# Performance work log

Hardware: AMD Instinct MI355X
Metric: run time of the kernel (lower is better)

Reference implementation:

```python
import jax, jax.numpy as jnp
import numpy as np


def setup_inputs() -> dict:
    key = jax.random.key(0)
    k1, k2, k3, k4, k5 = jax.random.split(key, 5)
    B, T, N, F, H = 32, 12, 512, 64, 64
    cat_x = jax.random.normal(k1, (B, T, N, F), dtype=jnp.float32)
    # Linear params (stored as [in, out]; torch stores [out, in] and does x @ W.T)
    lim = 1.0 / np.sqrt(F)
    Wq = jax.random.uniform(k2, (F, H), jnp.float32, -lim, lim)
    bq = jax.random.uniform(k3, (H,), jnp.float32, -lim, lim)
    Wk = jax.random.uniform(k4, (F, H), jnp.float32, -lim, lim)
    bk = jax.random.uniform(k5, (H,), jnp.float32, -lim, lim)
    return {"cat_x": cat_x, "Wq": Wq, "bq": bq, "Wk": Wk, "bk": bk, "tau": 4}


def reference(cat_x, Wq, bq, Wk, bk, tau):
    # cat_x: [B, T, N, F]
    q = cat_x @ Wq + bq  # [B, T, N, H]
    k = cat_x @ Wk + bk  # [B, T, N, H]
    qf = jnp.fft.rfft(q, axis=-1)  # [B, T, N, Fr]
    kf = jnp.fft.rfft(k, axis=-1)  # [B, T, N, Fr]
    # Vectorized over the original Python loop over i (query time step):
    # res[b, i, j, n, :] = qf[b, i, n, :] * conj(kf[b, j, n, :])
    res = qf[:, :, None, :, :] * jnp.conj(kf)[:, None, :, :, :]  # [B, Ti, Tj, N, Fr]
    corr = jnp.fft.irfft(res, axis=-1)  # [B, Ti, Tj, N, H] (H even -> exact round trip)
    # mean over batch, then hidden (last), then nodes == mean over (B, N, H)
    score_set = jnp.mean(corr, axis=(0, 3, 4))  # [Ti, Tj]
    scores, indices = jax.lax.top_k(score_set, tau)
    return scores, indices
```

## Files before the change

### kernel.cpp

```cpp
#include <hip/hip_runtime.h>

#define BB 32
#define TT 12
#define NN 512
#define FF 64
#define HH 64
#define NBLK 32
#define NCHUNK (NN / NBLK)
#define GRID (BB * NCHUNK)

#define WS_S  0
#define WS_WQ 144
#define WS_WK 208
#define WS_BQ 272
#define WS_BK 273

__global__ __launch_bounds__(384) void fft_sel_init(
    const float* __restrict__ Wq, const float* __restrict__ bq,
    const float* __restrict__ Wk, const float* __restrict__ bk,
    float* __restrict__ ws)
{
    const int tid = threadIdx.x;
    if (tid < TT * TT) {
        ws[WS_S + tid] = 0.f;
    } else if (tid >= 144 && tid < 144 + FF) {
        const int f = tid - 144;
        float a = 0.f;
        #pragma unroll
        for (int h = 0; h < HH; ++h) a += Wq[f * HH + h];
        ws[WS_WQ + f] = a;
    } else if (tid >= 208 && tid < 208 + FF) {
        const int f = tid - 208;
        float a = 0.f;
        #pragma unroll
        for (int h = 0; h < HH; ++h) a += Wk[f * HH + h];
        ws[WS_WK + f] = a;
    } else if (tid == 272) {
        float a = 0.f;
        #pragma unroll
        for (int h = 0; h < HH; ++h) a += bq[h];
        ws[WS_BQ] = a;
    } else if (tid == 273) {
        float a = 0.f;
        #pragma unroll
        for (int h = 0; h < HH; ++h) a += bk[h];
        ws[WS_BK] = a;
    }
}

__global__ __launch_bounds__(256) void fft_sel_main(
    const float* __restrict__ x,
    const float* __restrict__ ws,
    float* __restrict__ S)
{
    __shared__ float sq[TT][NBLK + 1];
    __shared__ float sk[TT][NBLK + 1];

    const int tid  = threadIdx.x;
    const int wave = tid >> 6;
    const int lane = tid & 63;
    const int sub  = lane >> 4;
    const int q    = lane & 15;

    const float4 wqv = *(const float4*)(ws + WS_WQ + 4 * q);
    const float4 wkv = *(const float4*)(ws + WS_WK + 4 * q);
    const float  bqs = ws[WS_BQ];
    const float  bks = ws[WS_BK];

    const int b  = blockIdx.x >> 4;
    const int n0 = (blockIdx.x & (NCHUNK - 1)) * NBLK;

    #pragma unroll
    for (int it = 0; it < (TT * NBLK) / 16; ++it) {
        const int r  = it * 16 + wave * 4 + sub;
        const int t  = r >> 5;
        const int nl = r & (NBLK - 1);
        const float4 v = *(const float4*)(x +
            (((size_t)b * TT + t) * NN + (n0 + nl)) * FF + q * 4);
        float pq = v.x * wqv.x + v.y * wqv.y + v.z * wqv.z + v.w * wqv.w;
        float pk = v.x * wkv.x + v.y * wkv.y + v.z * wkv.z + v.w * wkv.w;
        #pragma unroll
        for (int off = 1; off < 16; off <<= 1) {
            pq += __shfl_xor(pq, off);
            pk += __shfl_xor(pk, off);
        }
        if (q == 0) {
            sq[t][nl] = pq + bqs;
            sk[t][nl] = pk + bks;
        }
    }
    __syncthreads();

    if (tid < TT * TT) {
        const int i = tid / TT;
        const int j = tid % TT;
        float acc = 0.f;
        #pragma unroll
        for (int nl = 0; nl < NBLK; ++nl) acc += sq[i][nl] * sk[j][nl];
        atomicAdd(&S[tid], acc);
    }
}

__global__ void fft_sel_final(const float* __restrict__ S, float* __restrict__ out)
{
    const int i = threadIdx.x;
    if (i >= TT) return;
    const float scale = 1.0f / ((float)BB * (float)NN * (float)HH);
    float v[TT];
    bool used[TT];
    #pragma unroll
    for (int j = 0; j < TT; ++j) { v[j] = S[i * TT + j] * scale; used[j] = false; }
    #pragma unroll
    for (int s = 0; s < 4; ++s) {
        float best = -INFINITY;
        int bi = 0;
        for (int j = 0; j < TT; ++j) {
            if (!used[j] && v[j] > best) { best = v[j]; bi = j; }
        }
        used[bi] = true;
        out[i * 4 + s]          = best;
        out[TT * 4 + i * 4 + s] = (float)bi;
    }
}

extern "C" void kernel_launch(void* const* d_in, const int* in_sizes, int n_in,
                              void* d_out, int out_size, void* d_ws, size_t ws_size,
                              hipStream_t stream) {
    const float* x  = (const float*)d_in[0];
    const float* Wq = (const float*)d_in[1];
    const float* bq = (const float*)d_in[2];
    const float* Wk = (const float*)d_in[3];
    const float* bk = (const float*)d_in[4];
    float* ws = (float*)d_ws;

    fft_sel_init<<<1, 384, 0, stream>>>(Wq, bq, Wk, bk, ws);
    fft_sel_main<<<GRID, 256, 0, stream>>>(x, ws, ws + WS_S);
    fft_sel_final<<<1, 64, 0, stream>>>(ws + WS_S, (float*)d_out);
}
```

Measured before the change: 109.6 us.

## Shrink node chunk per block and spread atomics across shadow accumulators

Cuts the nodes per block from 32 to 8, so the grid grows from 512 to 2048 blocks. Each block now issues its 12 rows of loads in a flat, fully coalesced pattern across all 256 threads. To absorb the fourfold rise in atomic traffic on the 144 score cells, blocks add into one of 16 shadow copies, and the final kernel sums these before the top-k. The aim is more memory parallelism and latency hiding on a bandwidth-bound read of roughly 100MB, at the cost of more blocks and more atomics in total.

```diff
diff --git a/kernel.cpp b/kernel.cpp
--- a/kernel.cpp
+++ b/kernel.cpp
@@ -5,42 +5,43 @@
 #define NN 512
 #define FF 64
 #define HH 64
-#define NBLK 32
+#define NBLK 8
 #define NCHUNK (NN / NBLK)
 #define GRID (BB * NCHUNK)
+#define NSHADOW 16
 
-#define WS_S  0
-#define WS_WQ 144
-#define WS_WK 208
-#define WS_BQ 272
-#define WS_BK 273
+#define WS_SH 0
+#define WS_WQ (NSHADOW * TT * TT)
+#define WS_WK (WS_WQ + FF)
+#define WS_BQ (WS_WK + FF)
+#define WS_BK (WS_BQ + 1)
 
-__global__ __launch_bounds__(384) void fft_sel_init(
+__global__ __launch_bounds__(1024) void fft_sel_init(
     const float* __restrict__ Wq, const float* __restrict__ bq,
     const float* __restrict__ Wk, const float* __restrict__ bk,
     float* __restrict__ ws)
 {
     const int tid = threadIdx.x;
-    if (tid < TT * TT) {
-        ws[WS_S + tid] = 0.f;
-    } else if (tid >= 144 && tid < 144 + FF) {
-        const int f = tid - 144;
+    if (tid < 576) {
+        ((float4*)ws)[tid] = make_float4(0.f, 0.f, 0.f, 0.f);
+    } else if (tid < 576 + FF) {
+        const int f = tid - 576;
         float a = 0.f;
         #pragma unroll
         for (int h = 0; h < HH; ++h) a += Wq[f * HH + h];
         ws[WS_WQ + f] = a;
-    } else if (tid >= 208 && tid < 208 + FF) {
-        const int f = tid - 208;
+    } else if (tid < 576 + 2 * FF) {
+        const int f = tid - (576 + FF);
         float a = 0.f;
         #pragma unroll
         for (int h = 0; h < HH; ++h) a += Wk[f * HH + h];
         ws[WS_WK + f] = a;
-    } else if (tid == 272) {
+    } else if (tid == 576 + 2 * FF) {
         float a = 0.f;
         #pragma unroll
         for (int h = 0; h < HH; ++h) a += bq[h];
         ws[WS_BQ] = a;
-    } else if (tid == 273) {
+    } else if (tid == 576 + 2 * FF + 1) {
         float a = 0.f;
         #pragma unroll
         for (int h = 0; h < HH; ++h) a += bk[h];
@@ -48,33 +49,30 @@
     }
 }
 
-__global__ __launch_bounds__(256) void fft_sel_main(
+__global__ __launch_bounds__(256, 8) void fft_sel_main(
     const float* __restrict__ x,
-    const float* __restrict__ ws,
-    float* __restrict__ S)
+    const float* __restrict__ ws)
 {
-    __shared__ float sq[TT][NBLK + 1];
-    __shared__ float sk[TT][NBLK + 1];
+    __shared__ float sq[TT][NBLK];
+    __shared__ float sk[TT][NBLK];
 
-    const int tid  = threadIdx.x;
-    const int wave = tid >> 6;
-    const int lane = tid & 63;
-    const int sub  = lane >> 4;
-    const int q    = lane & 15;
+    const int tid = threadIdx.x;
+    const int q   = tid & 15;
 
     const float4 wqv = *(const float4*)(ws + WS_WQ + 4 * q);
     const float4 wkv = *(const float4*)(ws + WS_WK + 4 * q);
     const float  bqs = ws[WS_BQ];
     const float  bks = ws[WS_BK];
 
-    const int b  = blockIdx.x >> 4;
+    const int b  = blockIdx.x >> 6;
     const int n0 = (blockIdx.x & (NCHUNK - 1)) * NBLK;
 
     #pragma unroll
-    for (int it = 0; it < (TT * NBLK) / 16; ++it) {
-        const int r  = it * 16 + wave * 4 + sub;
-        const int t  = r >> 5;
-        const int nl = r & (NBLK - 1);
+    for (int it = 0; it < (TT * NBLK * 16) / 256; ++it) {
+        const int s   = it * 256 + tid;
+        const int row = s >> 4;
+        const int t   = row >> 3;
+        const int nl  = row & (NBLK - 1);
         const float4 v = *(const float4*)(x +
             (((size_t)b * TT + t) * NN + (n0 + nl)) * FF + q * 4);
         float pq = v.x * wqv.x + v.y * wqv.y + v.z * wqv.z + v.w * wqv.w;
@@ -97,29 +95,41 @@
         float acc = 0.f;
         #pragma unroll
         for (int nl = 0; nl < NBLK; ++nl) acc += sq[i][nl] * sk[j][nl];
+        float* S = (float*)ws + WS_SH + (blockIdx.x & (NSHADOW - 1)) * (TT * TT);
         atomicAdd(&S[tid], acc);
     }
 }
 
-__global__ void fft_sel_final(const float* __restrict__ S, float* __restrict__ out)
+__global__ __launch_bounds__(256) void fft_sel_final(
+    const float* __restrict__ ws, float* __restrict__ out)
 {
-    const int i = threadIdx.x;
-    if (i >= TT) return;
-    const float scale = 1.0f / ((float)BB * (float)NN * (float)HH);
-    float v[TT];
-    bool used[TT];
-    #pragma unroll
-    for (int j = 0; j < TT; ++j) { v[j] = S[i * TT + j] * scale; used[j] = false; }
-    #pragma unroll
-    for (int s = 0; s < 4; ++s) {
-        float best = -INFINITY;
-        int bi = 0;
-        for (int j = 0; j < TT; ++j) {
-            if (!used[j] && v[j] > best) { best = v[j]; bi = j; }
+    __shared__ float S[TT * TT];
+    const int tid = threadIdx.x;
+    if (tid < TT * TT) {
+        const float scale = 1.0f / ((float)BB * (float)NN * (float)HH);
+        float a = 0.f;
+        #pragma unroll
+        for (int c = 0; c < NSHADOW; ++c) a += ws[WS_SH + c * TT * TT + tid];
+        S[tid] = a * scale;
+    }
+    __syncthreads();
+    if (tid < TT) {
+        const int i = tid;
+        float v[TT];
+        bool used[TT];
+        #pragma unroll
+        for (int j = 0; j < TT; ++j) { v[j] = S[i * TT + j]; used[j] = false; }
+        #pragma unroll
+        for (int s = 0; s < 4; ++s) {
+            float best = -INFINITY;
+            int bi = 0;
+            for (int j = 0; j < TT; ++j) {
+                if (!used[j] && v[j] > best) { best = v[j]; bi = j; }
+            }
+            used[bi] = true;
+            out[i * 4 + s]          = best;
+            out[TT * 4 + i * 4 + s] = (float)bi;
         }
-        used[bi] = true;
-        out[i * 4 + s]          = best;
-        out[TT * 4 + i * 4 + s] = (float)bi;
     }
 }
 
@@ -133,7 +143,7 @@
     const float* bk = (const float*)d_in[4];
     float* ws = (float*)d_ws;
 
-    fft_sel_init<<<1, 384, 0, stream>>>(Wq, bq, Wk, bk, ws);
-    fft_sel_main<<<GRID, 256, 0, stream>>>(x, ws, ws + WS_S);
-    fft_sel_final<<<1, 64, 0, stream>>>(ws + WS_S, (float*)d_out);
+    fft_sel_init<<<1, 1024, 0, stream>>>(Wq, bq, Wk, bk, ws);
+    fft_sel_main<<<GRID, 256, 0, stream>>>(x, ws);
+    fft_sel_final<<<1, 256, 0, stream>>>(ws, (float*)d_out);
 }
```

New measurement: 97.72 us. -10.9%, faster.
